# Kernel optimization log

Measured on AMD Instinct MI355X. Metric: run time of the kernel, lower is better.

## Reference

```python
import jax, jax.numpy as jnp
import numpy as np

D_ATT = 256
D_GROUP = 32
N_GROUP = D_ATT // D_GROUP


def setup_inputs() -> dict:
    key = jax.random.key(0)
    ks = jax.random.split(key, 6)
    B, L = 4, 512
    import math
    s = 1.0 / math.sqrt(D_ATT)
    return {
        "x": jax.random.normal(ks[0], (B, L, D_ATT), dtype=jnp.float32),
        "Wq": jax.random.normal(ks[1], (D_ATT, D_ATT), dtype=jnp.float32) * s * 0.06,
        "Wk": jax.random.normal(ks[2], (D_ATT, D_ATT), dtype=jnp.float32) * s * 0.06,
        "Wv": jax.random.normal(ks[3], (D_ATT, D_ATT), dtype=jnp.float32) * s * 0.06,
        "w_mlp": jax.random.normal(ks[4], (D_GROUP,), dtype=jnp.float32) * 0.1,
        "b_mlp": jax.random.normal(ks[5], (1,), dtype=jnp.float32) * 0.1,
    }


def reference(x, Wq, Wk, Wv, w_mlp, b_mlp):
    B, L, d_att = x.shape
    G, Dg = N_GROUP, D_GROUP
    # nn.Linear(bias=False): y = x @ W.T
    Q = x @ Wq.T  # (B, L, d_att)
    K = x @ Wk.T
    V = x @ Wv.T
    Qg = Q.reshape(B, L, 1, G, Dg)
    Kg = K.reshape(B, 1, L, G, Dg)
    # group_MLP: ReLU -> Linear(Dg, 1) -> ReLU, applied to Q-K diff
    # diff: (B, Lq, Lk, G, Dg) -- the huge intermediate a fused kernel would avoid
    diff = Qg - Kg
    attn = jnp.einsum('bqkgd,d->bqkg', jax.nn.relu(diff), w_mlp) + b_mlp[0]
    attn = jax.nn.relu(attn)
    # positional_adding_bias=0, positional_multiplying_bias=1 (defaults), no mask
    attn = jax.nn.softmax(attn, axis=2)  # softmax over key positions
    # NOTE: original views V as (B, L, d_group, n_group) -- asymmetric grouping, kept faithful
    Vg = V.reshape(B, L, Dg, G)
    out = jnp.einsum('bqkg,bkdg->bqdg', attn, Vg)  # (B, Lq, Dg, G)
    return out.reshape(B, L, d_att)
```

## Files before the change

kernel.cpp:

```cpp
#include <hip/hip_runtime.h>

typedef float f32x2 __attribute__((ext_vector_type(2)));
typedef float f32x4 __attribute__((ext_vector_type(4)));

#define LL 512
#define M_ROWS 2048

__device__ __forceinline__ float quad_swap1(float x) {
    return __int_as_float(__builtin_amdgcn_mov_dpp(__float_as_int(x), 0xB1, 0xF, 0xF, true));
}
__device__ __forceinline__ float quad_swap2(float x) {
    return __int_as_float(__builtin_amdgcn_mov_dpp(__float_as_int(x), 0x4E, 0xF, 0xF, true));
}

__global__ __launch_bounds__(128) void qkv_gemm(
    const float* __restrict__ X, const float* __restrict__ Wq,
    const float* __restrict__ Wk, const float* __restrict__ Wv,
    float* __restrict__ Y)
{
    const int bx = blockIdx.x;
    const int by = blockIdx.y;
    const int mat = bx >> 2;
    const int n0 = (bx & 3) * 64;
    const int m0 = by * 32;
    const float* W = (mat == 0) ? Wq : (mat == 1 ? Wk : Wv);

    __shared__ float As[2][32][36];
    __shared__ float Bs[2][32][68];

    const int t = threadIdx.x;
    const int tx = t & 15;
    const int ty = t >> 4;

    int am[2], ak4[2];
#pragma unroll
    for (int r = 0; r < 2; ++r) { int idx = t + 128 * r; am[r] = idx >> 3; ak4[r] = idx & 7; }
    int bn[4], bk4[4]; size_t brow[4];
#pragma unroll
    for (int r = 0; r < 4; ++r) {
        int idx = t + 128 * r; bn[r] = idx >> 3; bk4[r] = idx & 7;
        int rowc = n0 + bn[r];
        brow[r] = (mat == 2) ? (size_t)(((rowc & 31) << 3) | (rowc >> 5)) : (size_t)rowc;
    }

    f32x4 arg[2], brg[4];
    auto load_tile = [&](int kc) {
#pragma unroll
        for (int r = 0; r < 2; ++r)
            arg[r] = *(const f32x4*)(X + (size_t)(m0 + am[r]) * 256 + kc + ak4[r] * 4);
#pragma unroll
        for (int r = 0; r < 4; ++r)
            brg[r] = *(const f32x4*)(W + brow[r] * 256 + kc + bk4[r] * 4);
    };
    auto store_tile = [&](int buf) {
#pragma unroll
        for (int r = 0; r < 2; ++r)
#pragma unroll
            for (int j = 0; j < 4; ++j) As[buf][ak4[r] * 4 + j][am[r]] = arg[r][j];
#pragma unroll
        for (int r = 0; r < 4; ++r)
#pragma unroll
            for (int j = 0; j < 4; ++j) Bs[buf][bk4[r] * 4 + j][bn[r]] = brg[r][j];
    };

    load_tile(0);
    store_tile(0);
    __syncthreads();

    f32x2 c[4][2];
#pragma unroll
    for (int i = 0; i < 4; ++i) { c[i][0] = (f32x2){0.f, 0.f}; c[i][1] = (f32x2){0.f, 0.f}; }

    for (int it = 0; it < 8; ++it) {
        const int buf = it & 1;
        if (it < 7) load_tile((it + 1) * 32);
#pragma unroll
        for (int kk = 0; kk < 32; ++kk) {
            const f32x4 a4 = *(const f32x4*)&As[buf][kk][ty * 4];
            const f32x4 b4 = *(const f32x4*)&Bs[buf][kk][tx * 4];
            const f32x2 bl = __builtin_shufflevector(b4, b4, 0, 1);
            const f32x2 bh = __builtin_shufflevector(b4, b4, 2, 3);
#pragma unroll
            for (int i = 0; i < 4; ++i) {
                const f32x2 ai = {a4[i], a4[i]};
                c[i][0] += ai * bl;
                c[i][1] += ai * bh;
            }
        }
        if (it < 7) {
            __syncthreads();
            store_tile(buf ^ 1);
            __syncthreads();
        }
    }

    float* Yb = Y + (size_t)mat * M_ROWS * 256;
#pragma unroll
    for (int i = 0; i < 4; ++i) {
        f32x4 v = {c[i][0].x, c[i][0].y, c[i][1].x, c[i][1].y};
        *(f32x4*)(Yb + (size_t)(m0 + ty * 4 + i) * 256 + n0 + tx * 4) = v;
    }
}

__global__ __launch_bounds__(512, 2) void attn_fused(
    const float* __restrict__ Y,
    const float* __restrict__ w_mlp, const float* __restrict__ b_mlp,
    float* __restrict__ out)
{
    const float* Qm = Y;
    const float* Km = Y + (size_t)M_ROWS * 256;
    const float* Vt = Y + (size_t)2 * M_ROWS * 256;

    const int bid = blockIdx.x;
    const int b = bid & 3;
    const int q0 = (bid >> 2) * 8;

    const int t = threadIdx.x;
    const int dh = t & 3;
    const int g = (t >> 2) & 7;
    const int p = t >> 5;
    const int lane32 = t & 31;

    __shared__ float accbuf[16][32][20];

    const int doff = g * 32 + dh * 8;
    const float bias = b_mlp[0];

    f32x2 w2[4];
    {
        f32x4 wa = *(const f32x4*)(w_mlp + dh * 8);
        f32x4 wb = *(const f32x4*)(w_mlp + dh * 8 + 4);
        w2[0] = __builtin_shufflevector(wa, wa, 0, 1);
        w2[1] = __builtin_shufflevector(wa, wa, 2, 3);
        w2[2] = __builtin_shufflevector(wb, wb, 0, 1);
        w2[3] = __builtin_shufflevector(wb, wb, 2, 3);
    }

    f32x2 qr2[8][4];
#pragma unroll
    for (int q = 0; q < 8; ++q) {
        const float* qp = Qm + ((size_t)(b * LL) + q0 + q) * 256 + doff;
        f32x4 qa = *(const f32x4*)qp;
        f32x4 qb = *(const f32x4*)(qp + 4);
        qr2[q][0] = __builtin_shufflevector(qa, qa, 0, 1);
        qr2[q][1] = __builtin_shufflevector(qa, qa, 2, 3);
        qr2[q][2] = __builtin_shufflevector(qb, qb, 0, 1);
        qr2[q][3] = __builtin_shufflevector(qb, qb, 2, 3);
    }

    f32x2 acc2[8][4];
#pragma unroll
    for (int q = 0; q < 8; ++q)
#pragma unroll
        for (int j = 0; j < 4; ++j) acc2[q][j] = (f32x2){0.f, 0.f};
    float l[8] = {0.f, 0.f, 0.f, 0.f, 0.f, 0.f, 0.f, 0.f};

    const float* kptr = Km + ((size_t)(b * LL) + p) * 256 + doff;
    const float* vptr = Vt + ((size_t)(b * LL) + p) * 256 + doff;

    auto compute = [&](f32x4 ka, f32x4 kb, f32x4 va, f32x4 vb) {
        f32x2 k2[4] = {__builtin_shufflevector(ka, ka, 0, 1),
                       __builtin_shufflevector(ka, ka, 2, 3),
                       __builtin_shufflevector(kb, kb, 0, 1),
                       __builtin_shufflevector(kb, kb, 2, 3)};
        f32x2 v2[4] = {__builtin_shufflevector(va, va, 0, 1),
                       __builtin_shufflevector(va, va, 2, 3),
                       __builtin_shufflevector(vb, vb, 0, 1),
                       __builtin_shufflevector(vb, vb, 2, 3)};
        const f32x2 z2 = {0.f, 0.f};
#pragma unroll
        for (int q = 0; q < 8; ++q) {
            f32x2 s2 = z2;
#pragma unroll
            for (int j = 0; j < 4; ++j) {
                f32x2 d2 = qr2[q][j] - k2[j];
                f32x2 r2 = __builtin_elementwise_max(d2, z2);
                s2 += w2[j] * r2;
            }
            float s = s2.x + s2.y;
            s += quad_swap1(s);
            s += quad_swap2(s);
            s = fmaxf(s + bias, 0.f);
            const float e = __expf(s);
            l[q] += e;
            const f32x2 e2 = {e, e};
#pragma unroll
            for (int j = 0; j < 4; ++j) acc2[q][j] += e2 * v2[j];
        }
    };

    f32x4 ka = *(const f32x4*)kptr, kb = *(const f32x4*)(kptr + 4);
    f32x4 va = *(const f32x4*)vptr, vb = *(const f32x4*)(vptr + 4);
#pragma unroll 1
    for (int i = 0; i < 31; ++i) {
        kptr += 16 * 256; vptr += 16 * 256;
        f32x4 ka2 = *(const f32x4*)kptr, kb2 = *(const f32x4*)(kptr + 4);
        f32x4 va2 = *(const f32x4*)vptr, vb2 = *(const f32x4*)(vptr + 4);
        compute(ka, kb, va, vb);
        ka = ka2; kb = kb2; va = va2; vb = vb2;
    }
    compute(ka, kb, va, vb);

#pragma unroll 1
    for (int r = 0; r < 4; ++r) {
#pragma unroll
        for (int qq = 0; qq < 2; ++qq) {
            const int q = r * 2 + qq;
#pragma unroll
            for (int j = 0; j < 4; ++j)
                *(f32x2*)&accbuf[p][lane32][qq * 8 + j * 2] = acc2[q][j];
        }
        if (dh == 0) {
            accbuf[p][lane32][16] = l[r * 2];
            accbuf[p][lane32][17] = l[r * 2 + 1];
        }
        __syncthreads();
        {
            const int c = t & 255;
            const int qq = t >> 8;
            const int og = c & 7, od = c >> 3;
            const int ogd = og * 4 + (od >> 3), odd = od & 7;
            float s = 0.f, ls = 0.f;
#pragma unroll
            for (int pp = 0; pp < 16; ++pp) {
                s  += accbuf[pp][ogd][qq * 8 + odd];
                ls += accbuf[pp][og * 4][16 + qq];
            }
            out[((size_t)(b * LL) + q0 + r * 2 + qq) * 256 + c] = s / ls;
        }
        __syncthreads();
    }
}

extern "C" void kernel_launch(void* const* d_in, const int* in_sizes, int n_in,
                              void* d_out, int out_size, void* d_ws, size_t ws_size,
                              hipStream_t stream) {
    (void)in_sizes; (void)n_in; (void)out_size; (void)ws_size;
    const float* x     = (const float*)d_in[0];
    const float* Wq    = (const float*)d_in[1];
    const float* Wk    = (const float*)d_in[2];
    const float* Wv    = (const float*)d_in[3];
    const float* w_mlp = (const float*)d_in[4];
    const float* b_mlp = (const float*)d_in[5];
    float* outp = (float*)d_out;
    float* Y    = (float*)d_ws;

    qkv_gemm<<<dim3(12, 64), 128, 0, stream>>>(x, Wq, Wk, Wv, Y);
    attn_fused<<<dim3(256), 512, 0, stream>>>(Y, w_mlp, b_mlp, outp);
}
```

Before: 130.2 us.

## Use split-bf16 MFMA for QKV projection and halve attention block size

Replaces the fp32 SIMT QKV GEMM with a pre-pass that splits inputs and weights into bf16 hi/lo parts, then a bf16 MFMA GEMM over the concatenated K=768 (hi*hi + hi*lo + lo*hi) to keep near-fp32 accuracy. Separately, the attention kernel drops to 256 threads per block with 8 key partitions instead of 16, and does the cross-partition reduction in one pass with a separate sum for the softmax denominator. This trades an extra launch and workspace traffic for the split pass against cheaper GEMM math, and changes the attention kernel's occupancy and reduction structure.

```diff
diff --git a/kernel.cpp b/kernel.cpp
--- a/kernel.cpp
+++ b/kernel.cpp
@@ -2,9 +2,11 @@
 
 typedef float f32x2 __attribute__((ext_vector_type(2)));
 typedef float f32x4 __attribute__((ext_vector_type(4)));
+typedef short bf16x8 __attribute__((ext_vector_type(8)));
 
 #define LL 512
 #define M_ROWS 2048
+#define KC 768
 
 __device__ __forceinline__ float quad_swap1(float x) {
     return __int_as_float(__builtin_amdgcn_mov_dpp(__float_as_int(x), 0xB1, 0xF, 0xF, true));
@@ -13,96 +15,127 @@
     return __int_as_float(__builtin_amdgcn_mov_dpp(__float_as_int(x), 0x4E, 0xF, 0xF, true));
 }
 
-__global__ __launch_bounds__(128) void qkv_gemm(
+__device__ __forceinline__ unsigned short bf16_rtne(float x) {
+    unsigned u = __float_as_uint(x);
+    return (unsigned short)((u + 0x7fffu + ((u >> 16) & 1u)) >> 16);
+}
+__device__ __forceinline__ float bf16_to_f(unsigned short h) {
+    return __uint_as_float((unsigned)h << 16);
+}
+
+__global__ __launch_bounds__(64) void split_bf16(
     const float* __restrict__ X, const float* __restrict__ Wq,
     const float* __restrict__ Wk, const float* __restrict__ Wv,
+    unsigned short* __restrict__ Xc, unsigned short* __restrict__ Wc)
+{
+    const int row = blockIdx.x;
+    const int t = threadIdx.x;
+    const float* src;
+    unsigned short* hi1; unsigned short* hi2; unsigned short* lo1;
+    if (row < M_ROWS) {
+        src = X + (size_t)row * 256;
+        hi1 = Xc + (size_t)row * KC;
+        hi2 = hi1 + 256;
+        lo1 = hi1 + 512;
+    } else {
+        const int n = row - M_ROWS;
+        const int mat = n >> 8, c = n & 255;
+        const int srow = (mat == 2) ? (((c & 31) << 3) | (c >> 5)) : c;
+        src = (mat == 0 ? Wq : (mat == 1 ? Wk : Wv)) + (size_t)srow * 256;
+        hi1 = Wc + (size_t)n * KC;
+        lo1 = hi1 + 256;
+        hi2 = hi1 + 512;
+    }
+    const f32x4 v = *(const f32x4*)(src + t * 4);
+    ushort4 h, l;
+    h.x = bf16_rtne(v.x); h.y = bf16_rtne(v.y); h.z = bf16_rtne(v.z); h.w = bf16_rtne(v.w);
+    l.x = bf16_rtne(v.x - bf16_to_f(h.x));
+    l.y = bf16_rtne(v.y - bf16_to_f(h.y));
+    l.z = bf16_rtne(v.z - bf16_to_f(h.z));
+    l.w = bf16_rtne(v.w - bf16_to_f(h.w));
+    *(ushort4*)(hi1 + t * 4) = h;
+    *(ushort4*)(hi2 + t * 4) = h;
+    *(ushort4*)(lo1 + t * 4) = l;
+}
+
+__global__ __launch_bounds__(64) void qkv_mfma(
+    const unsigned short* __restrict__ Xc, const unsigned short* __restrict__ Wc,
     float* __restrict__ Y)
 {
-    const int bx = blockIdx.x;
-    const int by = blockIdx.y;
-    const int mat = bx >> 2;
-    const int n0 = (bx & 3) * 64;
-    const int m0 = by * 32;
-    const float* W = (mat == 0) ? Wq : (mat == 1 ? Wk : Wv);
-
-    __shared__ float As[2][32][36];
-    __shared__ float Bs[2][32][68];
-
-    const int t = threadIdx.x;
-    const int tx = t & 15;
-    const int ty = t >> 4;
-
-    int am[2], ak4[2];
-#pragma unroll
-    for (int r = 0; r < 2; ++r) { int idx = t + 128 * r; am[r] = idx >> 3; ak4[r] = idx & 7; }
-    int bn[4], bk4[4]; size_t brow[4];
-#pragma unroll
-    for (int r = 0; r < 4; ++r) {
-        int idx = t + 128 * r; bn[r] = idx >> 3; bk4[r] = idx & 7;
-        int rowc = n0 + bn[r];
-        brow[r] = (mat == 2) ? (size_t)(((rowc & 31) << 3) | (rowc >> 5)) : (size_t)rowc;
-    }
-
-    f32x4 arg[2], brg[4];
-    auto load_tile = [&](int kc) {
-#pragma unroll
-        for (int r = 0; r < 2; ++r)
-            arg[r] = *(const f32x4*)(X + (size_t)(m0 + am[r]) * 256 + kc + ak4[r] * 4);
-#pragma unroll
-        for (int r = 0; r < 4; ++r)
-            brg[r] = *(const f32x4*)(W + brow[r] * 256 + kc + bk4[r] * 4);
-    };
-    auto store_tile = [&](int buf) {
-#pragma unroll
-        for (int r = 0; r < 2; ++r)
-#pragma unroll
-            for (int j = 0; j < 4; ++j) As[buf][ak4[r] * 4 + j][am[r]] = arg[r][j];
-#pragma unroll
-        for (int r = 0; r < 4; ++r)
-#pragma unroll
-            for (int j = 0; j < 4; ++j) Bs[buf][bk4[r] * 4 + j][bn[r]] = brg[r][j];
-    };
-
-    load_tile(0);
-    store_tile(0);
-    __syncthreads();
-
-    f32x2 c[4][2];
-#pragma unroll
-    for (int i = 0; i < 4; ++i) { c[i][0] = (f32x2){0.f, 0.f}; c[i][1] = (f32x2){0.f, 0.f}; }
-
-    for (int it = 0; it < 8; ++it) {
-        const int buf = it & 1;
-        if (it < 7) load_tile((it + 1) * 32);
-#pragma unroll
-        for (int kk = 0; kk < 32; ++kk) {
-            const f32x4 a4 = *(const f32x4*)&As[buf][kk][ty * 4];
-            const f32x4 b4 = *(const f32x4*)&Bs[buf][kk][tx * 4];
-            const f32x2 bl = __builtin_shufflevector(b4, b4, 0, 1);
-            const f32x2 bh = __builtin_shufflevector(b4, b4, 2, 3);
+    const int bid = blockIdx.x;
+    const int m0 = (bid & 31) * 64;
+    const int n0 = (bid >> 5) * 64;
+    const int l = threadIdx.x;
+    const int lr = l & 15;
+    const int lk = (l >> 4) * 8;
+
+    size_t aoff[4], boff[4];
+#pragma unroll
+    for (int i = 0; i < 4; ++i) {
+        aoff[i] = (size_t)(m0 + i * 16 + lr) * KC + lk;
+        boff[i] = (size_t)(n0 + i * 16 + lr) * KC + lk;
+    }
+
+    f32x4 acc[4][4];
+#pragma unroll
+    for (int i = 0; i < 4; ++i)
+#pragma unroll
+        for (int j = 0; j < 4; ++j) acc[i][j] = (f32x4){0.f, 0.f, 0.f, 0.f};
+
+    bf16x8 A0[4], B0[4], A1[4], B1[4];
+#pragma unroll
+    for (int i = 0; i < 4; ++i) {
+        A0[i] = *(const bf16x8*)(Xc + aoff[i]);
+        B0[i] = *(const bf16x8*)(Wc + boff[i]);
+    }
+
+#pragma unroll 1
+    for (int it = 0; it < 24; it += 2) {
+        const int ks1 = (it + 1) * 32;
+#pragma unroll
+        for (int i = 0; i < 4; ++i) {
+            A1[i] = *(const bf16x8*)(Xc + aoff[i] + ks1);
+            B1[i] = *(const bf16x8*)(Wc + boff[i] + ks1);
+        }
+#pragma unroll
+        for (int ai = 0; ai < 4; ++ai)
+#pragma unroll
+            for (int bi = 0; bi < 4; ++bi)
+                acc[ai][bi] = __builtin_amdgcn_mfma_f32_16x16x32_bf16(
+                    A0[ai], B0[bi], acc[ai][bi], 0, 0, 0);
+        if (it + 2 < 24) {
+            const int ks2 = (it + 2) * 32;
 #pragma unroll
             for (int i = 0; i < 4; ++i) {
-                const f32x2 ai = {a4[i], a4[i]};
-                c[i][0] += ai * bl;
-                c[i][1] += ai * bh;
+                A0[i] = *(const bf16x8*)(Xc + aoff[i] + ks2);
+                B0[i] = *(const bf16x8*)(Wc + boff[i] + ks2);
             }
         }
-        if (it < 7) {
-            __syncthreads();
-            store_tile(buf ^ 1);
-            __syncthreads();
-        }
-    }
-
+#pragma unroll
+        for (int ai = 0; ai < 4; ++ai)
+#pragma unroll
+            for (int bi = 0; bi < 4; ++bi)
+                acc[ai][bi] = __builtin_amdgcn_mfma_f32_16x16x32_bf16(
+                    A1[ai], B1[bi], acc[ai][bi], 0, 0, 0);
+    }
+
+    const int mat = n0 >> 8;
     float* Yb = Y + (size_t)mat * M_ROWS * 256;
 #pragma unroll
-    for (int i = 0; i < 4; ++i) {
-        f32x4 v = {c[i][0].x, c[i][0].y, c[i][1].x, c[i][1].y};
-        *(f32x4*)(Yb + (size_t)(m0 + ty * 4 + i) * 256 + n0 + tx * 4) = v;
-    }
-}
-
-__global__ __launch_bounds__(512, 2) void attn_fused(
+    for (int ai = 0; ai < 4; ++ai)
+#pragma unroll
+        for (int bi = 0; bi < 4; ++bi) {
+            const int col = (n0 & 255) + bi * 16 + lr;
+#pragma unroll
+            for (int r = 0; r < 4; ++r) {
+                const int row = m0 + ai * 16 + (l >> 4) * 4 + r;
+                Yb[(size_t)row * 256 + col] = acc[ai][bi][r];
+            }
+        }
+}
+
+#define ACC_S 73
+__global__ __launch_bounds__(256, 1) void attn_fused(
     const float* __restrict__ Y,
     const float* __restrict__ w_mlp, const float* __restrict__ b_mlp,
     float* __restrict__ out)
@@ -119,9 +152,9 @@
     const int dh = t & 3;
     const int g = (t >> 2) & 7;
     const int p = t >> 5;
-    const int lane32 = t & 31;
-
-    __shared__ float accbuf[16][32][20];
+
+    __shared__ float accbuf[8][32][ACC_S];
+    __shared__ float ltot[8][8];
 
     const int doff = g * 32 + dh * 8;
     const float bias = b_mlp[0];
@@ -192,8 +225,8 @@
     f32x4 ka = *(const f32x4*)kptr, kb = *(const f32x4*)(kptr + 4);
     f32x4 va = *(const f32x4*)vptr, vb = *(const f32x4*)(vptr + 4);
 #pragma unroll 1
-    for (int i = 0; i < 31; ++i) {
-        kptr += 16 * 256; vptr += 16 * 256;
+    for (int i = 0; i < 63; ++i) {
+        kptr += 8 * 256; vptr += 8 * 256;
         f32x4 ka2 = *(const f32x4*)kptr, kb2 = *(const f32x4*)(kptr + 4);
         f32x4 va2 = *(const f32x4*)vptr, vb2 = *(const f32x4*)(vptr + 4);
         compute(ka, kb, va, vb);
@@ -201,34 +234,45 @@
     }
     compute(ka, kb, va, vb);
 
-#pragma unroll 1
-    for (int r = 0; r < 4; ++r) {
-#pragma unroll
-        for (int qq = 0; qq < 2; ++qq) {
-            const int q = r * 2 + qq;
+    {
+        float* rowp = &accbuf[p][g * 4 + dh][0];
+#pragma unroll
+        for (int q = 0; q < 8; ++q)
 #pragma unroll
             for (int j = 0; j < 4; ++j)
-                *(f32x2*)&accbuf[p][lane32][qq * 8 + j * 2] = acc2[q][j];
-        }
+                *(f32x2*)(rowp + q * 8 + j * 2) = acc2[q][j];
         if (dh == 0) {
-            accbuf[p][lane32][16] = l[r * 2];
-            accbuf[p][lane32][17] = l[r * 2 + 1];
-        }
-        __syncthreads();
-        {
-            const int c = t & 255;
-            const int qq = t >> 8;
-            const int og = c & 7, od = c >> 3;
-            const int ogd = og * 4 + (od >> 3), odd = od & 7;
-            float s = 0.f, ls = 0.f;
-#pragma unroll
-            for (int pp = 0; pp < 16; ++pp) {
-                s  += accbuf[pp][ogd][qq * 8 + odd];
-                ls += accbuf[pp][og * 4][16 + qq];
-            }
-            out[((size_t)(b * LL) + q0 + r * 2 + qq) * 256 + c] = s / ls;
-        }
-        __syncthreads();
+            float* lp = &accbuf[p][g * 4][64];
+#pragma unroll
+            for (int q = 0; q < 8; ++q) lp[q] = l[q];
+        }
+    }
+    __syncthreads();
+
+    if (t < 64) {
+        const int gg = t >> 3, qq = t & 7;
+        float s = 0.f;
+#pragma unroll
+        for (int pp = 0; pp < 8; ++pp) s += accbuf[pp][gg * 4][64 + qq];
+        ltot[gg][qq] = s;
+    }
+    __syncthreads();
+
+    {
+        const int q = t >> 5;
+        const int dval = t & 31;
+        const int dhh = dval >> 3, jj = dval & 7;
+        float res[8];
+#pragma unroll
+        for (int gg = 0; gg < 8; ++gg) {
+            float s = 0.f;
+#pragma unroll
+            for (int pp = 0; pp < 8; ++pp) s += accbuf[pp][gg * 4 + dhh][q * 8 + jj];
+            res[gg] = s / ltot[gg][q];
+        }
+        float* op = out + ((size_t)(b * LL) + q0 + q) * 256 + dval * 8;
+        *(f32x4*)op       = (f32x4){res[0], res[1], res[2], res[3]};
+        *(f32x4*)(op + 4) = (f32x4){res[4], res[5], res[6], res[7]};
     }
 }
 
@@ -243,8 +287,12 @@
     const float* w_mlp = (const float*)d_in[4];
     const float* b_mlp = (const float*)d_in[5];
     float* outp = (float*)d_out;
-    float* Y    = (float*)d_ws;
-
-    qkv_gemm<<<dim3(12, 64), 128, 0, stream>>>(x, Wq, Wk, Wv, Y);
-    attn_fused<<<dim3(256), 512, 0, stream>>>(Y, w_mlp, b_mlp, outp);
-}
+
+    float* Y = (float*)d_ws;
+    unsigned short* Xc = (unsigned short*)((char*)d_ws + (size_t)6291456);
+    unsigned short* Wc = (unsigned short*)((char*)d_ws + (size_t)6291456 + 3145728);
+
+    split_bf16<<<dim3(M_ROWS + 768), 64, 0, stream>>>(x, Wq, Wk, Wv, Xc, Wc);
+    qkv_mfma<<<dim3(384), 64, 0, stream>>>(Xc, Wc, Y);
+    attn_fused<<<dim3(256), 256, 0, stream>>>(Y, w_mlp, b_mlp, outp);
+}
```

After: 128.8 us. Within noise of the previous version (-1.1%).
